# Optimization experiments

Measured on AMD Instinct MI355X. Metric: run time of the kernel, lower is better.

Reference implementation:

```python
import jax, jax.numpy as jnp
import numpy as np

N, NV, E0, HID, L, H = 32768, 64, 524288, 128, 4, 8
D = HID // H  # 16
SCALE = 1.0 / float(np.sqrt(D))


def _segment_softmax(logits, seg, num_segments):
    # numerically stable softmax grouped by destination node (leading axis = edges)
    m = jax.ops.segment_max(logits, seg, num_segments=num_segments)
    m = jnp.where(jnp.isfinite(m), m, 0.0)  # guard empty segments
    e = jnp.exp(logits - m[seg])
    s = jax.ops.segment_sum(e, seg, num_segments=num_segments)
    return e / (s[seg] + 1e-16)


def _forward(ei0, ei1, x_op, x_v, Wk, bk, Wq, bq, Wv, bv, Wa, ba, skip,
             a_rel, m_rel, p_rel, jk_w_in, jk_b_in, jk_w_out, jk_b_out,
             nm_w0, nm_b0, nm_w1, nm_b1, nm_w2, nm_b2, nm_w3, nm_b3,
             nm_w4, nm_b4, nm_w5, nm_b5, nm_w6, nm_b6,
             gm_w0, gm_b0, gm_w1, gm_b1):
    s0, d0 = ei0[0], ei0[1]
    s1, d1 = ei1[0], ei1[1]
    nm_ws = (nm_w0, nm_w1, nm_w2, nm_w3, nm_w4, nm_w5, nm_w6)
    nm_bs = (nm_b0, nm_b1, nm_b2, nm_b3, nm_b4, nm_b5, nm_b6)
    proj = lambda x, W, b: (x @ W.T + b).reshape(x.shape[0], H, D)
    outs_v = []
    for l in range(L):  # HGTConv layers (node types: 0='op', 1='virtual_op')
        k_op = proj(x_op, Wk[l, 0], bk[l, 0])
        q_op = proj(x_op, Wq[l, 0], bq[l, 0])
        v_op = proj(x_op, Wv[l, 0], bv[l, 0])
        q_v = proj(x_v, Wq[l, 1], bq[l, 1])  # virtual nodes only receive messages
        # relation 0: op -> op
        k0 = jnp.einsum('nhd,hde->nhe', k_op, a_rel[l, 0])
        v0 = jnp.einsum('nhd,hde->nhe', v_op, m_rel[l, 0])
        lg0 = jnp.sum(q_op[d0] * k0[s0], -1) * p_rel[l, 0] * SCALE  # [E0, H]
        al0 = _segment_softmax(lg0, d0, N)
        agg_op = jax.ops.segment_sum(al0[..., None] * v0[s0], d0, num_segments=N).reshape(N, HID)
        # relation 1: op -> virtual_op
        k1 = jnp.einsum('nhd,hde->nhe', k_op, a_rel[l, 1])
        v1 = jnp.einsum('nhd,hde->nhe', v_op, m_rel[l, 1])
        lg1 = jnp.sum(q_v[d1] * k1[s1], -1) * p_rel[l, 1] * SCALE  # [E1, H]
        al1 = _segment_softmax(lg1, d1, NV)
        agg_v = jax.ops.segment_sum(al1[..., None] * v1[s1], d1, num_segments=NV).reshape(NV, HID)
        # target-specific output projection + sigmoid-gated skip (in == out channels)
        o_op = jax.nn.gelu(agg_op, approximate=False) @ Wa[l, 0].T + ba[l, 0]
        g = jax.nn.sigmoid(skip[l, 0])
        x_op = g * o_op + (1.0 - g) * x_op
        o_v = jax.nn.gelu(agg_v, approximate=False) @ Wa[l, 1].T + ba[l, 1]
        g = jax.nn.sigmoid(skip[l, 1])
        x_v = g * o_v + (1.0 - g) * x_v
        outs_v.append(x_v)
    # JK via MultiheadAttention: seq = L layers, batch = NV virtual nodes
    xs = jnp.stack(outs_v)  # [L, NV, HID]
    qkv = xs @ jk_w_in.T + jk_b_in
    q, k, v = jnp.split(qkv, 3, axis=-1)
    q = q.reshape(L, NV, H, D)
    k = k.reshape(L, NV, H, D)
    v = v.reshape(L, NV, H, D)
    attn = jax.nn.softmax(jnp.einsum('qbhd,kbhd->bhqk', q, k) * SCALE, axis=-1)
    o = jnp.einsum('bhqk,kbhd->qbhd', attn, v).reshape(L, NV, HID)
    o = o @ jk_w_out.T + jk_b_out
    h = o.sum(0)  # [NV, HID]; batch_size == NV (1 virtual node per graph)
    for w_, b_ in zip(nm_ws[:-1], nm_bs[:-1]):  # node MLP (GELU hidden layers)
        h = jax.nn.gelu(h @ w_.T + b_, approximate=False)
    h = h @ nm_ws[-1].T + nm_bs[-1]  # [NV, 1]
    h = jax.nn.gelu(h @ gm_w0.T + gm_b0, approximate=False)  # graph MLP
    h = h @ gm_w1.T + gm_b1  # [NV, 1]
    return h[:, 0]  # squeeze(1)


def setup_inputs() -> dict:
    key = jax.random.key(0)
    ks = iter(jax.random.split(key, 64))
    nk = lambda: next(ks)
    w = lambda shape, s: jax.random.normal(nk(), shape, jnp.float32) * s
    inp = {}
    inp['x_op'] = jax.random.normal(nk(), (N, HID), jnp.float32)
    inp['x_v'] = jax.random.normal(nk(), (NV, HID), jnp.float32)
    src0 = jax.random.randint(nk(), (E0,), 0, N, jnp.int32)
    dst0 = jax.random.randint(nk(), (E0,), 0, N, jnp.int32)
    inp['ei0'] = jnp.stack([src0, dst0])
    batch_op = jax.random.randint(nk(), (N,), 0, NV, jnp.int32)  # graph id of each op node
    inp['ei1'] = jnp.stack([jnp.arange(N, dtype=jnp.int32), batch_op])
    for nm in ('Wk', 'Wq', 'Wv', 'Wa'):
        inp[nm] = w((L, 2, HID, HID), 0.1)
    for nm in ('bk', 'bq', 'bv', 'ba'):
        inp[nm] = jnp.zeros((L, 2, HID), jnp.float32)
    inp['skip'] = jnp.ones((L, 2), jnp.float32)
    inp['a_rel'] = w((L, 2, H, D, D), 0.25)
    inp['m_rel'] = w((L, 2, H, D, D), 0.25)
    inp['p_rel'] = jnp.ones((L, 2, H), jnp.float32)
    inp['jk_w_in'] = w((3 * HID, HID), 0.1)
    inp['jk_b_in'] = jnp.zeros((3 * HID,), jnp.float32)
    inp['jk_w_out'] = w((HID, HID), 0.1)
    inp['jk_b_out'] = jnp.zeros((HID,), jnp.float32)
    dims = [128, 64, 32, 16, 8, 4, 2, 1]  # _get_mlp_layer_dims(128, 1) + final out
    for i in range(7):
        inp[f'nm_w{i}'] = w((dims[i + 1], dims[i]), (2.0 / dims[i]) ** 0.5)
        inp[f'nm_b{i}'] = jnp.zeros((dims[i + 1],), jnp.float32)
    inp['gm_w0'] = w((2, 1), 1.0)
    inp['gm_b0'] = jnp.zeros((2,), jnp.float32)
    inp['gm_w1'] = w((1, 2), 0.7)
    inp['gm_b1'] = jnp.zeros((1,), jnp.float32)
    return inp


def reference(x_op, x_v, ei0, ei1, Wk, bk, Wq, bq, Wv, bv, Wa, ba, skip,
              a_rel, m_rel, p_rel, jk_w_in, jk_b_in, jk_w_out, jk_b_out,
              nm_w0, nm_b0, nm_w1, nm_b1, nm_w2, nm_b2, nm_w3, nm_b3,
              nm_w4, nm_b4, nm_w5, nm_b5, nm_w6, nm_b6,
              gm_w0, gm_b0, gm_w1, gm_b1):
    return _forward(ei0, ei1, x_op, x_v, Wk, bk, Wq, bq, Wv, bv, Wa, ba, skip,
                    a_rel, m_rel, p_rel, jk_w_in, jk_b_in, jk_w_out, jk_b_out,
                    nm_w0, nm_b0, nm_w1, nm_b1, nm_w2, nm_b2, nm_w3, nm_b3,
                    nm_w4, nm_b4, nm_w5, nm_b5, nm_w6, nm_b6,
                    gm_w0, gm_b0, gm_w1, gm_b1)
```

## Files before the change

### kernel.cpp

```cpp
#include <hip/hip_runtime.h>

#define NN   32768
#define NV   64
#define E0E  524288
#define HID  128
#define NL   4
#define NH   8
#define DH   16
#define SCALE 0.25f
#define LDA  136
#define CAP0 64
#define CAP1 1024

typedef __attribute__((ext_vector_type(8))) short short8;
typedef __attribute__((ext_vector_type(4))) float f32x4;

__device__ __forceinline__ float gelu_f(float x) {
  return 0.5f * x * (1.0f + erff(x * 0.7071067811865475f));
}
__device__ __forceinline__ float sigmoid_f(float x) {
  return 1.0f / (1.0f + __expf(-x));
}
__device__ __forceinline__ unsigned short f2bf(float x) {
  unsigned u = __float_as_uint(x);
  return (unsigned short)((u + 0x7FFFu + ((u >> 16) & 1u)) >> 16);
}
__device__ __forceinline__ float bf2f(unsigned short h) {
  return __uint_as_float(((unsigned)h) << 16);
}
__device__ __forceinline__ unsigned short f2h(float x) {
  union { _Float16 h; unsigned short u; } cv;
  cv.h = (_Float16)x;
  return cv.u;
}
__device__ __forceinline__ float h2f(unsigned short u) {
  union { _Float16 h; unsigned short u; } cv;
  cv.u = u;
  return (float)cv.h;
}
__device__ __forceinline__ float f16lo(unsigned u) { return h2f((unsigned short)(u & 0xffffu)); }
__device__ __forceinline__ float f16hi(unsigned u) { return h2f((unsigned short)(u >> 16)); }

union SMu {
  struct { unsigned short Ah[64][LDA]; unsigned short Al[64][LDA]; } a;
  struct { float xr[HID]; float xn[HID]; } v;
};

__device__ __forceinline__ void stage_A(unsigned short Ah[][LDA], unsigned short Al[][LDA],
                                        int t, const float* __restrict__ A, int m0, int gelu) {
  #pragma unroll
  for (int i = 0; i < 8; ++i) {
    int idx = t + 256 * i;
    int m = idx >> 5, c4 = (idx & 31) * 4;
    float4 v = *(const float4*)(A + (size_t)(m0 + m) * HID + c4);
    if (gelu) { v.x = gelu_f(v.x); v.y = gelu_f(v.y); v.z = gelu_f(v.z); v.w = gelu_f(v.w); }
    unsigned short h0 = f2bf(v.x), h1 = f2bf(v.y), h2 = f2bf(v.z), h3 = f2bf(v.w);
    *(ushort4*)&Ah[m][c4] = make_ushort4(h0, h1, h2, h3);
    *(ushort4*)&Al[m][c4] = make_ushort4(f2bf(v.x - bf2f(h0)), f2bf(v.y - bf2f(h1)),
                                         f2bf(v.z - bf2f(h2)), f2bf(v.w - bf2f(h3)));
  }
}

__device__ __forceinline__ void mfma_pass(const unsigned short Ah[][LDA],
    const unsigned short Al[][LDA], int t, const unsigned short* __restrict__ Wf,
    f32x4 acc[2][4]) {
  const int w = t >> 6, lane = t & 63, c16 = lane & 15, quad = lane >> 4;
  #pragma unroll
  for (int ks = 0; ks < 4; ++ks) {
    short8 ah[4], al[4];
    #pragma unroll
    for (int s = 0; s < 4; ++s) {
      ah[s] = *(const short8*)&Ah[16 * s + c16][ks * 32 + quad * 8];
      al[s] = *(const short8*)&Al[16 * s + c16][ks * 32 + quad * 8];
    }
    #pragma unroll
    for (int j = 0; j < 2; ++j) {
      const unsigned short* bp = Wf + (size_t)(((2 * w + j) * 4 + ks) * 64 + lane) * 8;
      short8 bh = *(const short8*)bp;
      short8 bl = *(const short8*)(bp + 16384);
      #pragma unroll
      for (int s = 0; s < 4; ++s) {
        acc[j][s] = __builtin_amdgcn_mfma_f32_16x16x32_bf16(ah[s], bh, acc[j][s], 0, 0, 0);
        acc[j][s] = __builtin_amdgcn_mfma_f32_16x16x32_bf16(ah[s], bl, acc[j][s], 0, 0, 0);
        acc[j][s] = __builtin_amdgcn_mfma_f32_16x16x32_bf16(al[s], bh, acc[j][s], 0, 0, 0);
      }
    }
  }
}

__device__ __forceinline__ void proj_q(const unsigned short Ah[][LDA],
    const unsigned short Al[][LDA], int t, int m0,
    const unsigned short* __restrict__ WqF, const float* __restrict__ bq0,
    unsigned short* __restrict__ Pqh) {
  const int w = t >> 6, c16 = t & 15, quad = (t & 63) >> 4;
  f32x4 acc[2][4] = {};
  mfma_pass(Ah, Al, t, WqF, acc);
  #pragma unroll
  for (int j = 0; j < 2; ++j) {
    const int col = (2 * w + j) * 16 + c16;
    const float bb = bq0[col];
    #pragma unroll
    for (int s = 0; s < 4; ++s)
      #pragma unroll
      for (int r = 0; r < 4; ++r) {
        int m = m0 + 16 * s + quad * 4 + r;
        Pqh[(size_t)m * HID + col] = f2h(acc[j][s][r] + bb);
      }
  }
}

__device__ __forceinline__ void proj_kv(const unsigned short Ah[][LDA],
    const unsigned short Al[][LDA], int t, int m0,
    const unsigned short* __restrict__ WfK, const float* __restrict__ bK,
    const float* __restrict__ bV, unsigned int* __restrict__ dst) {
  const int w = t >> 6, c16 = t & 15, quad = (t & 63) >> 4;
  unsigned kp[2][4][2];
  {
    f32x4 accK[2][4] = {};
    mfma_pass(Ah, Al, t, WfK, accK);
    #pragma unroll
    for (int j = 0; j < 2; ++j) {
      const float bbk = bK[(2 * w + j) * 16 + c16];
      #pragma unroll
      for (int s = 0; s < 4; ++s)
        #pragma unroll
        for (int rr = 0; rr < 2; ++rr)
          kp[j][s][rr] = (unsigned)f2h(accK[j][s][2 * rr] + bbk)
                       | ((unsigned)f2h(accK[j][s][2 * rr + 1] + bbk) << 16);
    }
  }
  f32x4 accV[2][4] = {};
  mfma_pass(Ah, Al, t, WfK + 32768, accV);
  #pragma unroll
  for (int j = 0; j < 2; ++j) {
    const int col = (2 * w + j) * 16 + c16;
    const float bbv = bV[col];
    #pragma unroll
    for (int s = 0; s < 4; ++s)
      #pragma unroll
      for (int r = 0; r < 4; ++r) {
        int m = m0 + 16 * s + quad * 4 + r;
        unsigned pk = (kp[j][s][r >> 1] >> ((r & 1) * 16)) & 0xffffu;
        unsigned pv = (unsigned)f2h(accV[j][s][r] + bbv);
        dst[(size_t)m * HID + col] = pk | (pv << 16);
      }
  }
}

__global__ __launch_bounds__(256) void k_sf(
    const float* __restrict__ Wk, const float* __restrict__ Wv,
    const float* __restrict__ bk, const float* __restrict__ bv,
    const float* __restrict__ a_rel, const float* __restrict__ m_rel,
    const float* __restrict__ p_rel, const float* __restrict__ Wq,
    const float* __restrict__ Wa, float* __restrict__ CB,
    unsigned short* __restrict__ FW, int* __restrict__ cnt0, int* __restrict__ cnt1) {
  __shared__ float cwl[HID * HID];
  int m = blockIdx.x, t = threadIdx.x;
  if (m >= 24) {
    int i = (m - 24) * 256 + t;
    cnt0[i] = 0;
    if (m == 24 && t < NV) cnt1[t] = 0;
    return;
  }
  unsigned short* hi = FW + (size_t)m * 32768;
  unsigned short* lo = hi + 16384;
  if (m < 16) {
    int l = m >> 2, mat = m & 3;
    int rel = mat >> 1;
    int isK = ((mat & 1) == 0);
    const float* W  = (isK ? Wk : Wv) + (size_t)(l * 2) * HID * HID;
    const float* bb = (isK ? bk : bv) + (l * 2) * HID;
    const float* R  = (isK ? a_rel : m_rel) + (size_t)((l * 2 + rel) * NH) * DH * DH;
    for (int o = t; o < HID * HID; o += 256) {
      int j = o >> 7, c = o & 127;
      int h = j >> 4, e = j & 15;
      float sc = isK ? (p_rel[(l * 2 + rel) * NH + h] * SCALE) : 1.0f;
      float s = 0.f;
      #pragma unroll
      for (int d = 0; d < DH; ++d)
        s += W[(size_t)(h * DH + d) * HID + c] * R[h * 256 + d * 16 + e];
      cwl[j * HID + c] = s * sc;
    }
    if (t < HID) {
      int j = t, h = j >> 4, e = j & 15;
      float sc = isK ? (p_rel[(l * 2 + rel) * NH + h] * SCALE) : 1.0f;
      float s = 0.f;
      #pragma unroll
      for (int d = 0; d < DH; ++d) s += bb[h * DH + d] * R[h * 256 + d * 16 + e];
      CB[m * HID + j] = s * sc;
    }
    __syncthreads();
    for (int idx = t; idx < 16384; idx += 256) {
      int j = idx & 7, lane = (idx >> 3) & 63, ks = (idx >> 9) & 3, nt = idx >> 11;
      int n = nt * 16 + (lane & 15);
      int k = ks * 32 + (lane >> 4) * 8 + j;
      float x = cwl[n * HID + k];
      unsigned short h = f2bf(x);
      hi[idx] = h;
      lo[idx] = f2bf(x - bf2f(h));
    }
    return;
  }
  const float* src = (m < 20) ? (Wq + (size_t)((m - 16) * 2) * HID * HID)
                              : (Wa + (size_t)((m - 20) * 2) * HID * HID);
  for (int idx = t; idx < 16384; idx += 256) {
    int j = idx & 7, lane = (idx >> 3) & 63, ks = (idx >> 9) & 3, nt = idx >> 11;
    int n = nt * 16 + (lane & 15);
    int k = ks * 32 + (lane >> 4) * 8 + j;
    float x = src[(size_t)n * HID + k];
    unsigned short h = f2bf(x);
    hi[idx] = h;
    lo[idx] = f2bf(x - bf2f(h));
  }
}

struct PreArgs {
  const int *src0, *dst0, *src1, *dst1;
  int *cnt0, *cnt1, *colB0, *colB1;
  const float* x_op; const unsigned short* FW; const float *bq, *CB;
  unsigned short* Pqh; unsigned int *Pkv0, *Pkv1;
  const float *x_v, *Wq1, *bq1; float* qv;
};

__launch_bounds__(256)
__global__ void k_pre(PreArgs a) {
  __shared__ SMu sm;
  int bx = blockIdx.x, t = threadIdx.x;
  if (bx < E0E / 4096) {
    int base = bx * 4096 + t;
    #pragma unroll
    for (int i = 0; i < 16; ++i) {
      int e = base + i * 256;
      int d = a.dst0[e];
      int pos = atomicAdd(&a.cnt0[d], 1);
      if (pos < CAP0) a.colB0[((size_t)d << 6) + pos] = a.src0[e];
    }
    return;
  }
  bx -= E0E / 4096;
  if (bx < NN / 4096) {
    int base = bx * 4096 + t;
    #pragma unroll
    for (int i = 0; i < 16; ++i) {
      int e = base + i * 256;
      int d = a.dst1[e];
      int pos = atomicAdd(&a.cnt1[d], 1);
      if (pos < CAP1) a.colB1[((size_t)d << 10) + pos] = a.src1[e];
    }
    return;
  }
  bx -= NN / 4096;
  if (bx < 3 * (NN / 64)) {
    int y = bx >> 9, tile = bx & 511;
    int m0 = tile * 64;
    stage_A(sm.a.Ah, sm.a.Al, t, a.x_op, m0, 0);
    __syncthreads();
    if (y == 0)      proj_q (sm.a.Ah, sm.a.Al, t, m0, a.FW + (size_t)16 * 32768, a.bq, a.Pqh);
    else if (y == 1) proj_kv(sm.a.Ah, sm.a.Al, t, m0, a.FW, a.CB, a.CB + HID, a.Pkv0);
    else             proj_kv(sm.a.Ah, sm.a.Al, t, m0, a.FW + (size_t)2 * 32768,
                             a.CB + 2 * HID, a.CB + 3 * HID, a.Pkv1);
    return;
  }
  bx -= 3 * (NN / 64);
  if (t < HID) sm.v.xr[t] = a.x_v[bx * HID + t];
  __syncthreads();
  if (t < HID) {
    float s = a.bq1[t];
    const float4* wr = (const float4*)(a.Wq1 + (size_t)t * HID);
    const float4* xx = (const float4*)sm.v.xr;
    #pragma unroll 8
    for (int c = 0; c < HID / 4; ++c) {
      float4 w4 = wr[c], x4 = xx[c];
      s += x4.x * w4.x + x4.y * w4.y + x4.z * w4.z + x4.w * w4.w;
    }
    a.qv[bx * HID + t] = s;
  }
}

__launch_bounds__(256)
__global__ void k_edges(const unsigned int* __restrict__ Pq32,
                        const unsigned int* __restrict__ Pkv0,
                        const unsigned int* __restrict__ Pkv1,
                        const int* __restrict__ cnt0, const int* __restrict__ colB0,
                        float* __restrict__ agg, const float* __restrict__ qv,
                        const int* __restrict__ cnt1, const int* __restrict__ colB1,
                        float* __restrict__ part) {
  int lane = threadIdx.x & 63;
  if (blockIdx.x < NN / 4) {
    int n = blockIdx.x * 4 + (threadIdx.x >> 6);
    unsigned qp = Pq32[(size_t)n * 64 + lane];
    float qx = f16lo(qp), qy = f16hi(qp);
    int cnt = cnt0[n]; if (cnt > CAP0) cnt = CAP0;
    int e = n << 6, e1 = (n << 6) + cnt;
    float acc0 = 0.f, acc1 = 0.f, wsum = 0.f;
    for (; e + 8 <= e1; e += 8) {
      const uint2* r[8];
      #pragma unroll
      for (int u = 0; u < 8; ++u)
        r[u] = (const uint2*)(Pkv0 + ((size_t)colB0[e + u] << 7) + 2 * lane);
      uint2 kv[8];
      #pragma unroll
      for (int u = 0; u < 8; ++u) kv[u] = *r[u];
      float p[8];
      #pragma unroll
      for (int u = 0; u < 8; ++u)
        p[u] = qx * f16lo(kv[u].x) + qy * f16lo(kv[u].y);
      #pragma unroll
      for (int u = 0; u < 8; ++u) {
        p[u] += __shfl_xor(p[u], 1); p[u] += __shfl_xor(p[u], 2); p[u] += __shfl_xor(p[u], 4);
      }
      #pragma unroll
      for (int u = 0; u < 8; ++u) {
        float wg = __expf(p[u]);
        wsum += wg; acc0 += wg * f16hi(kv[u].x); acc1 += wg * f16hi(kv[u].y);
      }
    }
    for (; e < e1; ++e) {
      uint2 kv = *(const uint2*)(Pkv0 + ((size_t)colB0[e] << 7) + 2 * lane);
      float p = qx * f16lo(kv.x) + qy * f16lo(kv.y);
      p += __shfl_xor(p, 1); p += __shfl_xor(p, 2); p += __shfl_xor(p, 4);
      float wg = __expf(p);
      wsum += wg; acc0 += wg * f16hi(kv.x); acc1 += wg * f16hi(kv.y);
    }
    float inv = 1.0f / (wsum + 1e-16f);
    *(float2*)(agg + (size_t)n * HID + 2 * lane) = make_float2(acc0 * inv, acc1 * inv);
  } else {
    int b2 = blockIdx.x - NN / 4;
    int g = b2 >> 3, ch = b2 & 7;
    int w = threadIdx.x >> 6;
    int slot = ch * 4 + w;
    float2 q = *(const float2*)(qv + g * HID + 2 * lane);
    int tot = cnt1[g]; if (tot > CAP1) tot = CAP1;
    int base = g << 10;
    int len = (tot + 31) >> 5;
    int s0 = base + slot * len;
    int s1 = s0 + len; int lim = base + tot; if (s1 > lim) s1 = lim;
    float acc0 = 0.f, acc1 = 0.f, wsum = 0.f;
    int e = s0;
    for (; e + 4 <= s1; e += 4) {
      uint2 ka = *(const uint2*)(Pkv1 + ((size_t)colB1[e]     << 7) + 2 * lane);
      uint2 kb = *(const uint2*)(Pkv1 + ((size_t)colB1[e + 1] << 7) + 2 * lane);
      uint2 kc = *(const uint2*)(Pkv1 + ((size_t)colB1[e + 2] << 7) + 2 * lane);
      uint2 kd = *(const uint2*)(Pkv1 + ((size_t)colB1[e + 3] << 7) + 2 * lane);
      float pa = q.x * f16lo(ka.x) + q.y * f16lo(ka.y);
      float pb = q.x * f16lo(kb.x) + q.y * f16lo(kb.y);
      float pc = q.x * f16lo(kc.x) + q.y * f16lo(kc.y);
      float pd = q.x * f16lo(kd.x) + q.y * f16lo(kd.y);
      pa += __shfl_xor(pa, 1); pb += __shfl_xor(pb, 1); pc += __shfl_xor(pc, 1); pd += __shfl_xor(pd, 1);
      pa += __shfl_xor(pa, 2); pb += __shfl_xor(pb, 2); pc += __shfl_xor(pc, 2); pd += __shfl_xor(pd, 2);
      pa += __shfl_xor(pa, 4); pb += __shfl_xor(pb, 4); pc += __shfl_xor(pc, 4); pd += __shfl_xor(pd, 4);
      float wa = __expf(pa), wb = __expf(pb), wc = __expf(pc), wd = __expf(pd);
      wsum += (wa + wb) + (wc + wd);
      acc0 += wa * f16hi(ka.x) + wb * f16hi(kb.x) + wc * f16hi(kc.x) + wd * f16hi(kd.x);
      acc1 += wa * f16hi(ka.y) + wb * f16hi(kb.y) + wc * f16hi(kc.y) + wd * f16hi(kd.y);
    }
    for (; e < s1; ++e) {
      uint2 kv = *(const uint2*)(Pkv1 + ((size_t)colB1[e] << 7) + 2 * lane);
      float p = q.x * f16lo(kv.x) + q.y * f16lo(kv.y);
      p += __shfl_xor(p, 1); p += __shfl_xor(p, 2); p += __shfl_xor(p, 4);
      float ww = __expf(p);
      wsum += ww; acc0 += ww * f16hi(kv.x); acc1 += ww * f16hi(kv.y);
    }
    float* pp = part + (size_t)(g * 32 + slot) * 192;
    pp[lane] = acc0; pp[64 + lane] = acc1; pp[128 + lane] = wsum;
  }
}

struct PArgs {
  const float *agg; const unsigned short *WaF_l; const float *ba_l0, *skip_l0, *xold;
  float *xcur;
  const float *part, *Wa_l1, *ba_l1, *skip_l1, *xvold;
  float *xv, *outsv_l, *qv;
  const float *Wq_n1, *bq_n1;
  int do_qv;
};

__device__ __forceinline__ void vtail(SMu& sm, int t, int v, const PArgs& f) {
  if (t < 64) {
    float a0 = 0.f, a1 = 0.f, ws2 = 0.f;
    for (int s = 0; s < 32; ++s) {
      const float* p = f.part + (size_t)(v * 32 + s) * 192;
      a0 += p[t]; a1 += p[64 + t]; ws2 += p[128 + t];
    }
    float inv = 1.0f / (ws2 + 1e-16f);
    sm.v.xr[2 * t]     = gelu_f(a0 * inv);
    sm.v.xr[2 * t + 1] = gelu_f(a1 * inv);
  }
  __syncthreads();
  if (t < HID) {
    float s = f.ba_l1[t];
    const float4* wr = (const float4*)(f.Wa_l1 + (size_t)t * HID);
    const float4* xx = (const float4*)sm.v.xr;
    #pragma unroll 8
    for (int c = 0; c < HID / 4; ++c) {
      float4 w4 = wr[c], x4 = xx[c];
      s += x4.x * w4.x + x4.y * w4.y + x4.z * w4.z + x4.w * w4.w;
    }
    float gg = sigmoid_f(*f.skip_l1);
    float nv2 = gg * s + (1.f - gg) * f.xvold[v * HID + t];
    f.xv[v * HID + t] = nv2;
    f.outsv_l[v * HID + t] = nv2;
    sm.v.xn[t] = nv2;
  }
  __syncthreads();
  if (f.do_qv && t < HID) {
    float s = f.bq_n1[t];
    const float4* wr = (const float4*)(f.Wq_n1 + (size_t)t * HID);
    const float4* xx = (const float4*)sm.v.xn;
    #pragma unroll 8
    for (int c = 0; c < HID / 4; ++c) {
      float4 w4 = wr[c], x4 = xx[c];
      s += x4.x * w4.x + x4.y * w4.y + x4.z * w4.z + x4.w * w4.w;
    }
    f.qv[v * HID + t] = s;
  }
}

__launch_bounds__(256)
__global__ void k_post_a(PArgs f) {
  __shared__ SMu sm;
  const int t = threadIdx.x;
  int bx = blockIdx.x;
  if (bx >= NN / 64) { vtail(sm, t, bx - NN / 64, f); return; }
  const int m0 = bx * 64;
  stage_A(sm.a.Ah, sm.a.Al, t, f.agg, m0, 1);
  __syncthreads();
  f32x4 acc[2][4] = {};
  mfma_pass(sm.a.Ah, sm.a.Al, t, f.WaF_l, acc);
  const int w = t >> 6, c16 = t & 15, quad = (t & 63) >> 4;
  float g = sigmoid_f(*f.skip_l0), gm1 = 1.0f - g;
  #pragma unroll
  for (int j = 0; j < 2; ++j) {
    const int col = (2 * w + j) * 16 + c16;
    const float bb = f.ba_l0[col];
    #pragma unroll
    for (int s = 0; s < 4; ++s)
      #pragma unroll
      for (int r = 0; r < 4; ++r) {
        int lm = 16 * s + quad * 4 + r;
        float v = acc[j][s][r] + bb;
        f.xcur[(size_t)(m0 + lm) * HID + col] =
            g * v + gm1 * f.xold[(size_t)(m0 + lm) * HID + col];
      }
  }
}

__launch_bounds__(256)
__global__ void k_post_b(const float* __restrict__ X, const unsigned short* __restrict__ WqF,
                         const unsigned short* __restrict__ CWF,
                         const float* __restrict__ bq0, const float* __restrict__ CBl,
                         unsigned short* __restrict__ Pqh, unsigned int* __restrict__ Pkv0,
                         unsigned int* __restrict__ Pkv1, int y_base) {
  __shared__ SMu sm;
  const int t = threadIdx.x;
  int y = y_base + (blockIdx.x >> 9), tile = blockIdx.x & 511;
  int m0 = tile * 64;
  stage_A(sm.a.Ah, sm.a.Al, t, X, m0, 0);
  __syncthreads();
  if (y == 0)      proj_q (sm.a.Ah, sm.a.Al, t, m0, WqF, bq0, Pqh);
  else if (y == 1) proj_kv(sm.a.Ah, sm.a.Al, t, m0, CWF, CBl, CBl + HID, Pkv0);
  else             proj_kv(sm.a.Ah, sm.a.Al, t, m0, CWF + (size_t)2 * 32768,
                           CBl + 2 * HID, CBl + 3 * HID, Pkv1);
}

struct TailW {
  const float *win, *bin, *wout, *bout;
  const float *nw0, *nb0, *nw1, *nb1, *nw2, *nb2, *nw3, *nb3, *nw4, *nb4, *nw5, *nb5, *nw6, *nb6;
  const float *gw0, *gb0, *gw1, *gb1;
};

struct TailArgs {
  const unsigned int* Pkv1; const int *cnt1, *colB1;
  const float* qv;
  const float *Wa_l1, *ba_l1, *skip_l1, *xvold;
  const float* outsv;
  TailW tw;
  float* outp;
};

__launch_bounds__(256)
__global__ void k_tail(TailArgs a) {
  __shared__ float xs[4][HID], qq[4][HID], kk[4][HID], vv[4][HID], oo[4][HID];
  __shared__ float att[NH][4][4];
  __shared__ float hb[HID], tb[64];
  __shared__ float p0[4][64], p1[4][64], pw[4][64];
  int v = blockIdx.x, t = threadIdx.x;
  int w = t >> 6, lane = t & 63;
  {
    float2 q = *(const float2*)(a.qv + v * HID + 2 * lane);
    int tot = a.cnt1[v]; if (tot > CAP1) tot = CAP1;
    int base = v << 10;
    int len = (tot + 3) >> 2;
    int s0 = base + w * len;
    int s1 = s0 + len; int lim = base + tot; if (s1 > lim) s1 = lim;
    float acc0 = 0.f, acc1 = 0.f, wsum = 0.f;
    int e = s0;
    for (; e + 8 <= s1; e += 8) {
      uint2 kv[8];
      #pragma unroll
      for (int u = 0; u < 8; ++u)
        kv[u] = *(const uint2*)(a.Pkv1 + ((size_t)a.colB1[e + u] << 7) + 2 * lane);
      float p[8];
      #pragma unroll
      for (int u = 0; u < 8; ++u)
        p[u] = q.x * f16lo(kv[u].x) + q.y * f16lo(kv[u].y);
      #pragma unroll
      for (int u = 0; u < 8; ++u) {
        p[u] += __shfl_xor(p[u], 1); p[u] += __shfl_xor(p[u], 2); p[u] += __shfl_xor(p[u], 4);
      }
      #pragma unroll
      for (int u = 0; u < 8; ++u) {
        float wg = __expf(p[u]);
        wsum += wg; acc0 += wg * f16hi(kv[u].x); acc1 += wg * f16hi(kv[u].y);
      }
    }
    for (; e < s1; ++e) {
      uint2 kv = *(const uint2*)(a.Pkv1 + ((size_t)a.colB1[e] << 7) + 2 * lane);
      float p = q.x * f16lo(kv.x) + q.y * f16lo(kv.y);
      p += __shfl_xor(p, 1); p += __shfl_xor(p, 2); p += __shfl_xor(p, 4);
      float ww = __expf(p);
      wsum += ww; acc0 += ww * f16hi(kv.x); acc1 += ww * f16hi(kv.y);
    }
    p0[w][lane] = acc0; p1[w][lane] = acc1; pw[w][lane] = wsum;
  }
  __syncthreads();
  if (t < 64) {
    float a0 = p0[0][t] + p0[1][t] + p0[2][t] + p0[3][t];
    float a1 = p1[0][t] + p1[1][t] + p1[2][t] + p1[3][t];
    float ws = pw[0][t] + pw[1][t] + pw[2][t] + pw[3][t];
    float inv = 1.0f / (ws + 1e-16f);
    hb[2 * t]     = gelu_f(a0 * inv);
    hb[2 * t + 1] = gelu_f(a1 * inv);
  }
  __syncthreads();
  if (t < HID) {
    float s = a.ba_l1[t];
    const float4* wr = (const float4*)(a.Wa_l1 + (size_t)t * HID);
    const float4* xx = (const float4*)hb;
    #pragma unroll 8
    for (int c = 0; c < HID / 4; ++c) {
      float4 w4 = wr[c], x4 = xx[c];
      s += x4.x * w4.x + x4.y * w4.y + x4.z * w4.z + x4.w * w4.w;
    }
    float gg = sigmoid_f(*a.skip_l1);
    xs[3][t] = gg * s + (1.f - gg) * a.xvold[v * HID + t];
    for (int l = 0; l < 3; ++l) xs[l][t] = a.outsv[(size_t)(l * NV + v) * HID + t];
  }
  __syncthreads();
  const TailW& tw = a.tw;
  if (t < HID) {
    for (int l = 0; l < 4; ++l) {
      float sq = tw.bin[t], sk = tw.bin[t + 128], sv = tw.bin[t + 256];
      const float* wq = tw.win + (size_t)t * HID;
      const float* wk = tw.win + (size_t)(t + 128) * HID;
      const float* wv = tw.win + (size_t)(t + 256) * HID;
      for (int c = 0; c < HID; ++c) {
        float x = xs[l][c];
        sq += x * wq[c]; sk += x * wk[c]; sv += x * wv[c];
      }
      qq[l][t] = sq; kk[l][t] = sk; vv[l][t] = sv;
    }
  }
  __syncthreads();
  if (t < 128) {
    int h = t >> 4, ql = (t >> 2) & 3, kl = t & 3;
    float s = 0.f;
    #pragma unroll
    for (int d = 0; d < DH; ++d) s += qq[ql][h * DH + d] * kk[kl][h * DH + d];
    att[h][ql][kl] = s * SCALE;
  }
  __syncthreads();
  if (t < 32) {
    int h = t >> 2, ql = t & 3;
    float m = att[h][ql][0];
    for (int k2 = 1; k2 < 4; ++k2) m = fmaxf(m, att[h][ql][k2]);
    float e[4], s = 0.f;
    for (int k2 = 0; k2 < 4; ++k2) { e[k2] = __expf(att[h][ql][k2] - m); s += e[k2]; }
    for (int k2 = 0; k2 < 4; ++k2) att[h][ql][k2] = e[k2] / s;
  }
  __syncthreads();
  if (t < 128) {
    int h = t >> 4;
    #pragma unroll
    for (int ql = 0; ql < 4; ++ql) {
      float s = 0.f;
      #pragma unroll
      for (int kl = 0; kl < 4; ++kl) s += att[h][ql][kl] * vv[kl][t];
      oo[ql][t] = s;
    }
  }
  __syncthreads();
  if (t < 128) {
    float s = 0.f;
    const float* wr = tw.wout + (size_t)t * HID;
    for (int l = 0; l < 4; ++l) {
      float ss = tw.bout[t];
      for (int c = 0; c < HID; ++c) ss += oo[l][c] * wr[c];
      s += ss;
    }
    hb[t] = s;
  }
  __syncthreads();
  if (t < 64) { float s = tw.nb0[t]; const float* wr = tw.nw0 + t * 128; for (int c = 0; c < 128; ++c) s += hb[c] * wr[c]; tb[t] = gelu_f(s); }
  __syncthreads();
  if (t < 32) { float s = tw.nb1[t]; const float* wr = tw.nw1 + t * 64;  for (int c = 0; c < 64;  ++c) s += tb[c] * wr[c]; hb[t] = gelu_f(s); }
  __syncthreads();
  if (t < 16) { float s = tw.nb2[t]; const float* wr = tw.nw2 + t * 32;  for (int c = 0; c < 32;  ++c) s += hb[c] * wr[c]; tb[t] = gelu_f(s); }
  __syncthreads();
  if (t < 8)  { float s = tw.nb3[t]; const float* wr = tw.nw3 + t * 16;  for (int c = 0; c < 16;  ++c) s += tb[c] * wr[c]; hb[t] = gelu_f(s); }
  __syncthreads();
  if (t < 4)  { float s = tw.nb4[t]; const float* wr = tw.nw4 + t * 8;   for (int c = 0; c < 8;   ++c) s += hb[c] * wr[c]; tb[t] = gelu_f(s); }
  __syncthreads();
  if (t < 2)  { float s = tw.nb5[t]; const float* wr = tw.nw5 + t * 4;   for (int c = 0; c < 4;   ++c) s += tb[c] * wr[c]; hb[t] = gelu_f(s); }
  __syncthreads();
  if (t == 0) {
    float s = hb[0] * tw.nw6[0] + hb[1] * tw.nw6[1] + tw.nb6[0];
    float g0 = gelu_f(s * tw.gw0[0] + tw.gb0[0]);
    float g1 = gelu_f(s * tw.gw0[1] + tw.gb0[1]);
    a.outp[v] = g0 * tw.gw1[0] + g1 * tw.gw1[1] + tw.gb1[0];
  }
}

extern "C" void kernel_launch(void* const* d_in, const int* in_sizes, int n_in,
                              void* d_out, int out_size, void* d_ws, size_t ws_size,
                              hipStream_t stream) {
  const float* x_op = (const float*)d_in[0];
  const float* x_v  = (const float*)d_in[1];
  const int*   ei0  = (const int*)d_in[2];
  const int*   ei1  = (const int*)d_in[3];
  const float* Wk   = (const float*)d_in[4];
  const float* Wq   = (const float*)d_in[5];
  const float* Wv   = (const float*)d_in[6];
  const float* Wa   = (const float*)d_in[7];
  const float* bk   = (const float*)d_in[8];
  const float* bq   = (const float*)d_in[9];
  const float* bv   = (const float*)d_in[10];
  const float* ba   = (const float*)d_in[11];
  const float* skip = (const float*)d_in[12];
  const float* a_rel = (const float*)d_in[13];
  const float* m_rel = (const float*)d_in[14];
  const float* p_rel = (const float*)d_in[15];
  (void)in_sizes; (void)n_in; (void)out_size; (void)ws_size;

  char* wsp = (char*)d_ws;
  size_t off = 0;
  auto alloc = [&](size_t bytes) -> void* {
    void* p = wsp + off;
    off += (bytes + 255) & ~(size_t)255;
    return p;
  };
  unsigned short* Pqh = (unsigned short*)alloc((size_t)NN * HID * 2);
  unsigned int* Pkv0 = (unsigned int*)alloc((size_t)NN * HID * 4);
  unsigned int* Pkv1 = (unsigned int*)alloc((size_t)NN * HID * 4);
  float* xopA  = (float*)alloc((size_t)NN * HID * 4);
  float* xopB  = (float*)alloc((size_t)NN * HID * 4);
  float* agg   = (float*)alloc((size_t)NN * HID * 4);
  float* CB    = (float*)alloc((size_t)16 * HID * 4);
  unsigned short* FW = (unsigned short*)alloc((size_t)24 * 32768 * 2);
  float* xv    = (float*)alloc((size_t)NV * HID * 4);
  float* qv    = (float*)alloc((size_t)NV * HID * 4);
  float* outsv = (float*)alloc((size_t)NL * NV * HID * 4);
  float* part  = (float*)alloc((size_t)NV * 32 * 192 * 4);
  int* cnt0    = (int*)alloc((size_t)NN * 4);
  int* colB0   = (int*)alloc((size_t)NN * CAP0 * 4);
  int* cnt1    = (int*)alloc((size_t)NV * 4);
  int* colB1   = (int*)alloc((size_t)NV * CAP1 * 4);

  k_sf<<<24 + NN / 256, 256, 0, stream>>>(Wk, Wv, bk, bv, a_rel, m_rel, p_rel, Wq, Wa,
                                          CB, FW, cnt0, cnt1);

  PreArgs pa;
  pa.src0 = ei0; pa.dst0 = ei0 + E0E;
  pa.src1 = ei1; pa.dst1 = ei1 + NN;
  pa.cnt0 = cnt0; pa.cnt1 = cnt1; pa.colB0 = colB0; pa.colB1 = colB1;
  pa.x_op = x_op; pa.FW = FW; pa.bq = bq; pa.CB = CB;
  pa.Pqh = Pqh; pa.Pkv0 = Pkv0; pa.Pkv1 = Pkv1;
  pa.x_v = x_v; pa.Wq1 = Wq + (size_t)1 * HID * HID; pa.bq1 = bq + HID; pa.qv = qv;
  k_pre<<<E0E / 4096 + NN / 4096 + 3 * (NN / 64) + NV, 256, 0, stream>>>(pa);

  for (int l = 0; l < NL - 1; ++l) {
    k_edges<<<NN / 4 + NV * 8, 256, 0, stream>>>((const unsigned int*)Pqh, Pkv0, Pkv1,
                                                 cnt0, colB0, agg, qv, cnt1, colB1, part);
    float* xold = (l == 0) ? (float*)x_op : ((l & 1) ? xopA : xopB);
    float* xcur = (l & 1) ? xopB : xopA;
    PArgs f;
    f.agg = agg;
    f.WaF_l = FW + (size_t)(20 + l) * 32768;
    f.ba_l0 = ba + (l * 2 + 0) * HID;
    f.skip_l0 = skip + l * 2 + 0;
    f.xold = xold;
    f.xcur = xcur;
    f.part = part;
    f.Wa_l1 = Wa + (size_t)(l * 2 + 1) * HID * HID;
    f.ba_l1 = ba + (l * 2 + 1) * HID;
    f.skip_l1 = skip + l * 2 + 1;
    f.xvold = (l == 0) ? x_v : xv;
    f.xv = xv;
    f.outsv_l = outsv + (size_t)l * NV * HID;
    f.qv = qv;
    int ln = l + 1;
    f.Wq_n1 = Wq + (size_t)(ln * 2 + 1) * HID * HID;
    f.bq_n1 = bq + (ln * 2 + 1) * HID;
    f.do_qv = 1;
    k_post_a<<<NN / 64 + NV, 256, 0, stream>>>(f);
    int nsl = (l < 2) ? 3 : 1;
    int yb  = (l < 2) ? 0 : 2;
    k_post_b<<<nsl * (NN / 64), 256, 0, stream>>>(
        xcur, FW + (size_t)(16 + ln) * 32768, FW + (size_t)(ln * 4) * 32768,
        bq + (size_t)ln * 2 * HID, CB + (size_t)ln * 4 * HID, Pqh, Pkv0, Pkv1, yb);
  }

  TailArgs ta;
  ta.Pkv1 = Pkv1; ta.cnt1 = cnt1; ta.colB1 = colB1;
  ta.qv = qv;
  ta.Wa_l1 = Wa + (size_t)(3 * 2 + 1) * HID * HID;
  ta.ba_l1 = ba + (3 * 2 + 1) * HID;
  ta.skip_l1 = skip + 3 * 2 + 1;
  ta.xvold = xv;
  ta.outsv = outsv;
  ta.tw.win  = (const float*)d_in[16]; ta.tw.bin  = (const float*)d_in[17];
  ta.tw.wout = (const float*)d_in[18]; ta.tw.bout = (const float*)d_in[19];
  ta.tw.nw0 = (const float*)d_in[20]; ta.tw.nb0 = (const float*)d_in[21];
  ta.tw.nw1 = (const float*)d_in[22]; ta.tw.nb1 = (const float*)d_in[23];
  ta.tw.nw2 = (const float*)d_in[24]; ta.tw.nb2 = (const float*)d_in[25];
  ta.tw.nw3 = (const float*)d_in[26]; ta.tw.nb3 = (const float*)d_in[27];
  ta.tw.nw4 = (const float*)d_in[28]; ta.tw.nb4 = (const float*)d_in[29];
  ta.tw.nw5 = (const float*)d_in[30]; ta.tw.nb5 = (const float*)d_in[31];
  ta.tw.nw6 = (const float*)d_in[32]; ta.tw.nb6 = (const float*)d_in[33];
  ta.tw.gw0 = (const float*)d_in[34]; ta.tw.gb0 = (const float*)d_in[35];
  ta.tw.gw1 = (const float*)d_in[36]; ta.tw.gb1 = (const float*)d_in[37];
  ta.outp = (float*)d_out;
  k_tail<<<NV, 256, 0, stream>>>(ta);
}
```

Measured before the change: 548.9 us.

## Fuse edge aggregation with output projection and move virtual tail into projection kernel

```diff
diff --git a/kernel.cpp b/kernel.cpp
--- a/kernel.cpp
+++ b/kernel.cpp
@@ -277,60 +277,26 @@
   }
 }
 
+struct LArgs {
+  const unsigned int *Pq32, *Pkv0, *Pkv1;
+  const int *cnt0, *colB0, *cnt1, *colB1;
+  const float* qv;
+  const unsigned short* WaF_l; const float *ba_l0, *skip_l0, *xold;
+  float *xcur;
+  float* part;
+};
+
 __launch_bounds__(256)
-__global__ void k_edges(const unsigned int* __restrict__ Pq32,
-                        const unsigned int* __restrict__ Pkv0,
-                        const unsigned int* __restrict__ Pkv1,
-                        const int* __restrict__ cnt0, const int* __restrict__ colB0,
-                        float* __restrict__ agg, const float* __restrict__ qv,
-                        const int* __restrict__ cnt1, const int* __restrict__ colB1,
-                        float* __restrict__ part) {
-  int lane = threadIdx.x & 63;
-  if (blockIdx.x < NN / 4) {
-    int n = blockIdx.x * 4 + (threadIdx.x >> 6);
-    unsigned qp = Pq32[(size_t)n * 64 + lane];
-    float qx = f16lo(qp), qy = f16hi(qp);
-    int cnt = cnt0[n]; if (cnt > CAP0) cnt = CAP0;
-    int e = n << 6, e1 = (n << 6) + cnt;
-    float acc0 = 0.f, acc1 = 0.f, wsum = 0.f;
-    for (; e + 8 <= e1; e += 8) {
-      const uint2* r[8];
-      #pragma unroll
-      for (int u = 0; u < 8; ++u)
-        r[u] = (const uint2*)(Pkv0 + ((size_t)colB0[e + u] << 7) + 2 * lane);
-      uint2 kv[8];
-      #pragma unroll
-      for (int u = 0; u < 8; ++u) kv[u] = *r[u];
-      float p[8];
-      #pragma unroll
-      for (int u = 0; u < 8; ++u)
-        p[u] = qx * f16lo(kv[u].x) + qy * f16lo(kv[u].y);
-      #pragma unroll
-      for (int u = 0; u < 8; ++u) {
-        p[u] += __shfl_xor(p[u], 1); p[u] += __shfl_xor(p[u], 2); p[u] += __shfl_xor(p[u], 4);
-      }
-      #pragma unroll
-      for (int u = 0; u < 8; ++u) {
-        float wg = __expf(p[u]);
-        wsum += wg; acc0 += wg * f16hi(kv[u].x); acc1 += wg * f16hi(kv[u].y);
-      }
-    }
-    for (; e < e1; ++e) {
-      uint2 kv = *(const uint2*)(Pkv0 + ((size_t)colB0[e] << 7) + 2 * lane);
-      float p = qx * f16lo(kv.x) + qy * f16lo(kv.y);
-      p += __shfl_xor(p, 1); p += __shfl_xor(p, 2); p += __shfl_xor(p, 4);
-      float wg = __expf(p);
-      wsum += wg; acc0 += wg * f16hi(kv.x); acc1 += wg * f16hi(kv.y);
-    }
-    float inv = 1.0f / (wsum + 1e-16f);
-    *(float2*)(agg + (size_t)n * HID + 2 * lane) = make_float2(acc0 * inv, acc1 * inv);
-  } else {
-    int b2 = blockIdx.x - NN / 4;
+__global__ void k_layer(LArgs a) {
+  __shared__ SMu sm;
+  int bx = blockIdx.x, t = threadIdx.x;
+  int w = t >> 6, lane = t & 63;
+  if (bx >= NN / 64) {
+    int b2 = bx - NN / 64;
     int g = b2 >> 3, ch = b2 & 7;
-    int w = threadIdx.x >> 6;
     int slot = ch * 4 + w;
-    float2 q = *(const float2*)(qv + g * HID + 2 * lane);
-    int tot = cnt1[g]; if (tot > CAP1) tot = CAP1;
+    float2 q = *(const float2*)(a.qv + g * HID + 2 * lane);
+    int tot = a.cnt1[g]; if (tot > CAP1) tot = CAP1;
     int base = g << 10;
     int len = (tot + 31) >> 5;
     int s0 = base + slot * len;
@@ -338,10 +304,10 @@
     float acc0 = 0.f, acc1 = 0.f, wsum = 0.f;
     int e = s0;
     for (; e + 4 <= s1; e += 4) {
-      uint2 ka = *(const uint2*)(Pkv1 + ((size_t)colB1[e]     << 7) + 2 * lane);
-      uint2 kb = *(const uint2*)(Pkv1 + ((size_t)colB1[e + 1] << 7) + 2 * lane);
-      uint2 kc = *(const uint2*)(Pkv1 + ((size_t)colB1[e + 2] << 7) + 2 * lane);
-      uint2 kd = *(const uint2*)(Pkv1 + ((size_t)colB1[e + 3] << 7) + 2 * lane);
+      uint2 ka = *(const uint2*)(a.Pkv1 + ((size_t)a.colB1[e]     << 7) + 2 * lane);
+      uint2 kb = *(const uint2*)(a.Pkv1 + ((size_t)a.colB1[e + 1] << 7) + 2 * lane);
+      uint2 kc = *(const uint2*)(a.Pkv1 + ((size_t)a.colB1[e + 2] << 7) + 2 * lane);
+      uint2 kd = *(const uint2*)(a.Pkv1 + ((size_t)a.colB1[e + 3] << 7) + 2 * lane);
       float pa = q.x * f16lo(ka.x) + q.y * f16lo(ka.y);
       float pb = q.x * f16lo(kb.x) + q.y * f16lo(kb.y);
       float pc = q.x * f16lo(kc.x) + q.y * f16lo(kc.y);
@@ -355,112 +321,142 @@
       acc1 += wa * f16hi(ka.y) + wb * f16hi(kb.y) + wc * f16hi(kc.y) + wd * f16hi(kd.y);
     }
     for (; e < s1; ++e) {
-      uint2 kv = *(const uint2*)(Pkv1 + ((size_t)colB1[e] << 7) + 2 * lane);
+      uint2 kv = *(const uint2*)(a.Pkv1 + ((size_t)a.colB1[e] << 7) + 2 * lane);
       float p = q.x * f16lo(kv.x) + q.y * f16lo(kv.y);
       p += __shfl_xor(p, 1); p += __shfl_xor(p, 2); p += __shfl_xor(p, 4);
       float ww = __expf(p);
       wsum += ww; acc0 += ww * f16hi(kv.x); acc1 += ww * f16hi(kv.y);
     }
-    float* pp = part + (size_t)(g * 32 + slot) * 192;
+    float* pp = a.part + (size_t)(g * 32 + slot) * 192;
     pp[lane] = acc0; pp[64 + lane] = acc1; pp[128 + lane] = wsum;
-  }
-}
-
-struct PArgs {
-  const float *agg; const unsigned short *WaF_l; const float *ba_l0, *skip_l0, *xold;
-  float *xcur;
+    return;
+  }
+  const int m0 = bx * 64;
+  for (int i = 0; i < 16; ++i) {
+    int lm = w * 16 + i;
+    int n = m0 + lm;
+    unsigned qp = a.Pq32[(size_t)n * 64 + lane];
+    float qx = f16lo(qp), qy = f16hi(qp);
+    int cnt = a.cnt0[n]; if (cnt > CAP0) cnt = CAP0;
+    int e = n << 6, e1 = (n << 6) + cnt;
+    float acc0 = 0.f, acc1 = 0.f, wsum = 0.f;
+    for (; e + 8 <= e1; e += 8) {
+      uint2 kv[8];
+      #pragma unroll
+      for (int u = 0; u < 8; ++u)
+        kv[u] = *(const uint2*)(a.Pkv0 + ((size_t)a.colB0[e + u] << 7) + 2 * lane);
+      float p[8];
+      #pragma unroll
+      for (int u = 0; u < 8; ++u)
+        p[u] = qx * f16lo(kv[u].x) + qy * f16lo(kv[u].y);
+      #pragma unroll
+      for (int u = 0; u < 8; ++u) {
+        p[u] += __shfl_xor(p[u], 1); p[u] += __shfl_xor(p[u], 2); p[u] += __shfl_xor(p[u], 4);
+      }
+      #pragma unroll
+      for (int u = 0; u < 8; ++u) {
+        float wg = __expf(p[u]);
+        wsum += wg; acc0 += wg * f16hi(kv[u].x); acc1 += wg * f16hi(kv[u].y);
+      }
+    }
+    for (; e < e1; ++e) {
+      uint2 kv = *(const uint2*)(a.Pkv0 + ((size_t)a.colB0[e] << 7) + 2 * lane);
+      float p = qx * f16lo(kv.x) + qy * f16lo(kv.y);
+      p += __shfl_xor(p, 1); p += __shfl_xor(p, 2); p += __shfl_xor(p, 4);
+      float wg = __expf(p);
+      wsum += wg; acc0 += wg * f16hi(kv.x); acc1 += wg * f16hi(kv.y);
+    }
+    float inv = 1.0f / (wsum + 1e-16f);
+    float v0 = gelu_f(acc0 * inv), v1 = gelu_f(acc1 * inv);
+    unsigned short h0 = f2bf(v0), h1 = f2bf(v1);
+    *(unsigned*)&sm.a.Ah[lm][2 * lane] = (unsigned)h0 | ((unsigned)h1 << 16);
+    *(unsigned*)&sm.a.Al[lm][2 * lane] =
+        (unsigned)f2bf(v0 - bf2f(h0)) | ((unsigned)f2bf(v1 - bf2f(h1)) << 16);
+  }
+  __syncthreads();
+  f32x4 acc[2][4] = {};
+  mfma_pass(sm.a.Ah, sm.a.Al, t, a.WaF_l, acc);
+  const int c16 = t & 15, quad = (t & 63) >> 4;
+  float g = sigmoid_f(*a.skip_l0), gm1 = 1.0f - g;
+  #pragma unroll
+  for (int j = 0; j < 2; ++j) {
+    const int col = (2 * w + j) * 16 + c16;
+    const float bb = a.ba_l0[col];
+    #pragma unroll
+    for (int s = 0; s < 4; ++s)
+      #pragma unroll
+      for (int r = 0; r < 4; ++r) {
+        int lm = 16 * s + quad * 4 + r;
+        float v = acc[j][s][r] + bb;
+        a.xcur[(size_t)(m0 + lm) * HID + col] =
+            g * v + gm1 * a.xold[(size_t)(m0 + lm) * HID + col];
+      }
+  }
+}
+
+struct BArgs {
+  const float* X; const unsigned short *WqF, *CWF; const float *bq0, *CBl;
+  unsigned short* Pqh; unsigned int *Pkv0, *Pkv1; int y_base, nsl;
   const float *part, *Wa_l1, *ba_l1, *skip_l1, *xvold;
   float *xv, *outsv_l, *qv;
-  const float *Wq_n1, *bq_n1;
-  int do_qv;
+  const float *Wq_n1, *bq_n1; int do_qv;
 };
 
-__device__ __forceinline__ void vtail(SMu& sm, int t, int v, const PArgs& f) {
-  if (t < 64) {
-    float a0 = 0.f, a1 = 0.f, ws2 = 0.f;
-    for (int s = 0; s < 32; ++s) {
-      const float* p = f.part + (size_t)(v * 32 + s) * 192;
-      a0 += p[t]; a1 += p[64 + t]; ws2 += p[128 + t];
-    }
-    float inv = 1.0f / (ws2 + 1e-16f);
-    sm.v.xr[2 * t]     = gelu_f(a0 * inv);
-    sm.v.xr[2 * t + 1] = gelu_f(a1 * inv);
-  }
-  __syncthreads();
-  if (t < HID) {
-    float s = f.ba_l1[t];
-    const float4* wr = (const float4*)(f.Wa_l1 + (size_t)t * HID);
-    const float4* xx = (const float4*)sm.v.xr;
-    #pragma unroll 8
-    for (int c = 0; c < HID / 4; ++c) {
-      float4 w4 = wr[c], x4 = xx[c];
-      s += x4.x * w4.x + x4.y * w4.y + x4.z * w4.z + x4.w * w4.w;
-    }
-    float gg = sigmoid_f(*f.skip_l1);
-    float nv2 = gg * s + (1.f - gg) * f.xvold[v * HID + t];
-    f.xv[v * HID + t] = nv2;
-    f.outsv_l[v * HID + t] = nv2;
-    sm.v.xn[t] = nv2;
-  }
-  __syncthreads();
-  if (f.do_qv && t < HID) {
-    float s = f.bq_n1[t];
-    const float4* wr = (const float4*)(f.Wq_n1 + (size_t)t * HID);
-    const float4* xx = (const float4*)sm.v.xn;
-    #pragma unroll 8
-    for (int c = 0; c < HID / 4; ++c) {
-      float4 w4 = wr[c], x4 = xx[c];
-      s += x4.x * w4.x + x4.y * w4.y + x4.z * w4.z + x4.w * w4.w;
-    }
-    f.qv[v * HID + t] = s;
-  }
-}
-
 __launch_bounds__(256)
-__global__ void k_post_a(PArgs f) {
+__global__ void k_post_b(BArgs b) {
   __shared__ SMu sm;
   const int t = threadIdx.x;
   int bx = blockIdx.x;
-  if (bx >= NN / 64) { vtail(sm, t, bx - NN / 64, f); return; }
-  const int m0 = bx * 64;
-  stage_A(sm.a.Ah, sm.a.Al, t, f.agg, m0, 1);
-  __syncthreads();
-  f32x4 acc[2][4] = {};
-  mfma_pass(sm.a.Ah, sm.a.Al, t, f.WaF_l, acc);
-  const int w = t >> 6, c16 = t & 15, quad = (t & 63) >> 4;
-  float g = sigmoid_f(*f.skip_l0), gm1 = 1.0f - g;
-  #pragma unroll
-  for (int j = 0; j < 2; ++j) {
-    const int col = (2 * w + j) * 16 + c16;
-    const float bb = f.ba_l0[col];
-    #pragma unroll
-    for (int s = 0; s < 4; ++s)
-      #pragma unroll
-      for (int r = 0; r < 4; ++r) {
-        int lm = 16 * s + quad * 4 + r;
-        float v = acc[j][s][r] + bb;
-        f.xcur[(size_t)(m0 + lm) * HID + col] =
-            g * v + gm1 * f.xold[(size_t)(m0 + lm) * HID + col];
-      }
-  }
-}
-
-__launch_bounds__(256)
-__global__ void k_post_b(const float* __restrict__ X, const unsigned short* __restrict__ WqF,
-                         const unsigned short* __restrict__ CWF,
-                         const float* __restrict__ bq0, const float* __restrict__ CBl,
-                         unsigned short* __restrict__ Pqh, unsigned int* __restrict__ Pkv0,
-                         unsigned int* __restrict__ Pkv1, int y_base) {
-  __shared__ SMu sm;
-  const int t = threadIdx.x;
-  int y = y_base + (blockIdx.x >> 9), tile = blockIdx.x & 511;
+  if (bx >= b.nsl * (NN / 64)) {
+    int v = bx - b.nsl * (NN / 64);
+    if (t < 64) {
+      float a0 = 0.f, a1 = 0.f, ws2 = 0.f;
+      for (int s = 0; s < 32; ++s) {
+        const float* p = b.part + (size_t)(v * 32 + s) * 192;
+        a0 += p[t]; a1 += p[64 + t]; ws2 += p[128 + t];
+      }
+      float inv = 1.0f / (ws2 + 1e-16f);
+      sm.v.xr[2 * t]     = gelu_f(a0 * inv);
+      sm.v.xr[2 * t + 1] = gelu_f(a1 * inv);
+    }
+    __syncthreads();
+    if (t < HID) {
+      float s = b.ba_l1[t];
+      const float4* wr = (const float4*)(b.Wa_l1 + (size_t)t * HID);
+      const float4* xx = (const float4*)sm.v.xr;
+      #pragma unroll 8
+      for (int c = 0; c < HID / 4; ++c) {
+        float4 w4 = wr[c], x4 = xx[c];
+        s += x4.x * w4.x + x4.y * w4.y + x4.z * w4.z + x4.w * w4.w;
+      }
+      float gg = sigmoid_f(*b.skip_l1);
+      float nv2 = gg * s + (1.f - gg) * b.xvold[v * HID + t];
+      b.xv[v * HID + t] = nv2;
+      b.outsv_l[v * HID + t] = nv2;
+      sm.v.xn[t] = nv2;
+    }
+    __syncthreads();
+    if (b.do_qv && t < HID) {
+      float s = b.bq_n1[t];
+      const float4* wr = (const float4*)(b.Wq_n1 + (size_t)t * HID);
+      const float4* xx = (const float4*)sm.v.xn;
+      #pragma unroll 8
+      for (int c = 0; c < HID / 4; ++c) {
+        float4 w4 = wr[c], x4 = xx[c];
+        s += x4.x * w4.x + x4.y * w4.y + x4.z * w4.z + x4.w * w4.w;
+      }
+      b.qv[v * HID + t] = s;
+    }
+    return;
+  }
+  int y = b.y_base + (bx >> 9), tile = bx & 511;
   int m0 = tile * 64;
-  stage_A(sm.a.Ah, sm.a.Al, t, X, m0, 0);
-  __syncthreads();
-  if (y == 0)      proj_q (sm.a.Ah, sm.a.Al, t, m0, WqF, bq0, Pqh);
-  else if (y == 1) proj_kv(sm.a.Ah, sm.a.Al, t, m0, CWF, CBl, CBl + HID, Pkv0);
-  else             proj_kv(sm.a.Ah, sm.a.Al, t, m0, CWF + (size_t)2 * 32768,
-                           CBl + 2 * HID, CBl + 3 * HID, Pkv1);
+  stage_A(sm.a.Ah, sm.a.Al, t, b.X, m0, 0);
+  __syncthreads();
+  if (y == 0)      proj_q (sm.a.Ah, sm.a.Al, t, m0, b.WqF, b.bq0, b.Pqh);
+  else if (y == 1) proj_kv(sm.a.Ah, sm.a.Al, t, m0, b.CWF, b.CBl, b.CBl + HID, b.Pkv0);
+  else             proj_kv(sm.a.Ah, sm.a.Al, t, m0, b.CWF + (size_t)2 * 32768,
+                           b.CBl + 2 * HID, b.CBl + 3 * HID, b.Pkv1);
 }
 
 struct TailW {
@@ -654,7 +650,6 @@
   unsigned int* Pkv1 = (unsigned int*)alloc((size_t)NN * HID * 4);
   float* xopA  = (float*)alloc((size_t)NN * HID * 4);
   float* xopB  = (float*)alloc((size_t)NN * HID * 4);
-  float* agg   = (float*)alloc((size_t)NN * HID * 4);
   float* CB    = (float*)alloc((size_t)16 * HID * 4);
   unsigned short* FW = (unsigned short*)alloc((size_t)24 * 32768 * 2);
   float* xv    = (float*)alloc((size_t)NV * HID * 4);
@@ -679,35 +674,41 @@
   k_pre<<<E0E / 4096 + NN / 4096 + 3 * (NN / 64) + NV, 256, 0, stream>>>(pa);
 
   for (int l = 0; l < NL - 1; ++l) {
-    k_edges<<<NN / 4 + NV * 8, 256, 0, stream>>>((const unsigned int*)Pqh, Pkv0, Pkv1,
-                                                 cnt0, colB0, agg, qv, cnt1, colB1, part);
     float* xold = (l == 0) ? (float*)x_op : ((l & 1) ? xopA : xopB);
     float* xcur = (l & 1) ? xopB : xopA;
-    PArgs f;
-    f.agg = agg;
-    f.WaF_l = FW + (size_t)(20 + l) * 32768;
-    f.ba_l0 = ba + (l * 2 + 0) * HID;
-    f.skip_l0 = skip + l * 2 + 0;
-    f.xold = xold;
-    f.xcur = xcur;
-    f.part = part;
-    f.Wa_l1 = Wa + (size_t)(l * 2 + 1) * HID * HID;
-    f.ba_l1 = ba + (l * 2 + 1) * HID;
-    f.skip_l1 = skip + l * 2 + 1;
-    f.xvold = (l == 0) ? x_v : xv;
-    f.xv = xv;
-    f.outsv_l = outsv + (size_t)l * NV * HID;
-    f.qv = qv;
+    LArgs la;
+    la.Pq32 = (const unsigned int*)Pqh; la.Pkv0 = Pkv0; la.Pkv1 = Pkv1;
+    la.cnt0 = cnt0; la.colB0 = colB0; la.cnt1 = cnt1; la.colB1 = colB1;
+    la.qv = qv;
+    la.WaF_l = FW + (size_t)(20 + l) * 32768;
+    la.ba_l0 = ba + (l * 2 + 0) * HID;
+    la.skip_l0 = skip + l * 2 + 0;
+    la.xold = xold;
+    la.xcur = xcur;
+    la.part = part;
+    k_layer<<<NN / 64 + NV * 8, 256, 0, stream>>>(la);
     int ln = l + 1;
-    f.Wq_n1 = Wq + (size_t)(ln * 2 + 1) * HID * HID;
-    f.bq_n1 = bq + (ln * 2 + 1) * HID;
-    f.do_qv = 1;
-    k_post_a<<<NN / 64 + NV, 256, 0, stream>>>(f);
-    int nsl = (l < 2) ? 3 : 1;
-    int yb  = (l < 2) ? 0 : 2;
-    k_post_b<<<nsl * (NN / 64), 256, 0, stream>>>(
-        xcur, FW + (size_t)(16 + ln) * 32768, FW + (size_t)(ln * 4) * 32768,
-        bq + (size_t)ln * 2 * HID, CB + (size_t)ln * 4 * HID, Pqh, Pkv0, Pkv1, yb);
+    BArgs b;
+    b.X = xcur;
+    b.WqF = FW + (size_t)(16 + ln) * 32768;
+    b.CWF = FW + (size_t)(ln * 4) * 32768;
+    b.bq0 = bq + (size_t)ln * 2 * HID;
+    b.CBl = CB + (size_t)ln * 4 * HID;
+    b.Pqh = Pqh; b.Pkv0 = Pkv0; b.Pkv1 = Pkv1;
+    b.y_base = (l < 2) ? 0 : 2;
+    b.nsl    = (l < 2) ? 3 : 1;
+    b.part = part;
+    b.Wa_l1 = Wa + (size_t)(l * 2 + 1) * HID * HID;
+    b.ba_l1 = ba + (l * 2 + 1) * HID;
+    b.skip_l1 = skip + l * 2 + 1;
+    b.xvold = (l == 0) ? x_v : xv;
+    b.xv = xv;
+    b.outsv_l = outsv + (size_t)l * NV * HID;
+    b.qv = qv;
+    b.Wq_n1 = Wq + (size_t)(ln * 2 + 1) * HID * HID;
+    b.bq_n1 = bq + (ln * 2 + 1) * HID;
+    b.do_qv = 1;
+    k_post_b<<<b.nsl * (NN / 64) + NV, 256, 0, stream>>>(b);
   }
 
   TailArgs ta;
```

Measured after the change: 683.0 us. 24.4% more time.
